# Kernel tuning notes

Measured on AMD Instinct MI355X. Metric: run time of the kernel, lower is better.

Reference implementation:

```python
import jax, jax.numpy as jnp
import numpy as np


def setup_inputs() -> dict:
    key = jax.random.key(0)
    k1, k2 = jax.random.split(key)
    B, N, T, D = 4, 5000, 96, 64
    spatial_nodes = jax.random.normal(k1, (B, N, D), dtype=jnp.float32)
    temporal_nodes = jax.random.normal(k2, (B, T, D), dtype=jnp.float32)
    return {"spatial_nodes": spatial_nodes, "temporal_nodes": temporal_nodes}


def reference(spatial_nodes, temporal_nodes):
    # node_embs: [B, N+T, D]
    node_embs = jnp.concatenate([spatial_nodes, temporal_nodes], axis=1)
    # Gram matrix per batch: [B, N+T, N+T]
    adj = jax.nn.relu(jnp.einsum('bnf,bmf->bnm', node_embs, node_embs))
    M = node_embs.shape[1]
    eye = jnp.eye(M, dtype=adj.dtype)  # broadcast over batch instead of repeat
    adj = jnp.tanh(adj + eye)
    # NOTE: the torch original additionally extracts per-batch edge lists via
    # adj[bi].nonzero() — a data-dependent-shape compaction that is not
    # jit-expressible; the dense adj carries identical information
    # (edge (i,j) exists iff adj[b,i,j] != 0, weight = adj[b,i,j]).
    return adj
```

## Files before the change

kernel.cpp:

```cpp
#include <hip/hip_runtime.h>


#define NSP 5000
#define NTM 96
#define MM  5096
#define DD  64
#define BT  128
#define NTILE 40

typedef __attribute__((ext_vector_type(8))) short short8;
typedef __attribute__((ext_vector_type(8))) unsigned short ushort8;
typedef __attribute__((ext_vector_type(4))) float f32x4;

#define OFF_RH 0u
#define OFF_RL 16384u
#define OFF_CH 32768u
#define OFF_CL 49152u

__device__ __forceinline__ unsigned short bf16_rn(float x) {
  unsigned u = __float_as_uint(x);
  u += 0x7FFFu + ((u >> 16) & 1u);
  return (unsigned short)(u >> 16);
}
__device__ __forceinline__ float bf16_f32(unsigned short s) {
  return __uint_as_float(((unsigned)s) << 16);
}

__global__ __launch_bounds__(256) void stg_adj_kernel(
    const float* __restrict__ sp, const float* __restrict__ tm,
    float* __restrict__ out) {
  __shared__ unsigned char lds[65536];
  const int bi = blockIdx.x;
  const int bj = blockIdx.y;
  const int b  = blockIdx.z;
  const int t  = threadIdx.x;

  {
    const int r = t >> 1;
    const int h = t & 1;
    #pragma unroll
    for (int side = 0; side < 2; ++side) {
      const int tbase = (side == 0 ? bi : bj) * BT;
      unsigned char* dh = lds + (side == 0 ? OFF_RH : OFF_CH);
      unsigned char* dl = lds + (side == 0 ? OFF_RL : OFF_CL);
      const int g = tbase + r;
      float f[32];
      if (g < MM) {
        const float* src = (g < NSP)
            ? sp + ((size_t)b * NSP + g) * DD + h * 32
            : tm + ((size_t)b * NTM + (g - NSP)) * DD + h * 32;
        const float4* s4 = reinterpret_cast<const float4*>(src);
        #pragma unroll
        for (int i = 0; i < 8; ++i) {
          float4 v = s4[i];
          f[4*i+0] = v.x; f[4*i+1] = v.y; f[4*i+2] = v.z; f[4*i+3] = v.w;
        }
      } else {
        #pragma unroll
        for (int i = 0; i < 32; ++i) f[i] = 0.f;
      }
      #pragma unroll
      for (int c = 0; c < 4; ++c) {
        ushort8 H, L;
        #pragma unroll
        for (int i = 0; i < 8; ++i) {
          const float x = f[8*c + i];
          const unsigned short hi = bf16_rn(x);
          H[i] = (unsigned short)hi;
          L[i] = bf16_rn(x - bf16_f32(hi));
        }
        const unsigned slot = (unsigned)(h * 4 + c);
        const unsigned byte = (unsigned)(r << 7) + ((slot << 4) ^ (((unsigned)(r & 7)) << 4));
        *reinterpret_cast<ushort8*>(dh + byte) = H;
        *reinterpret_cast<ushort8*>(dl + byte) = L;
      }
    }
  }
  __syncthreads();

  const int lane = t & 63;
  const int wave = t >> 6;
  const int wr = (wave >> 1) << 6;
  const int wc = (wave & 1) << 6;
  const int lr = lane & 15;
  const int lg = lane >> 4;

  f32x4 acc[4][4];
  #pragma unroll
  for (int m = 0; m < 4; ++m)
    #pragma unroll
    for (int n = 0; n < 4; ++n)
      acc[m][n] = (f32x4){0.f, 0.f, 0.f, 0.f};

  #pragma unroll
  for (int ks = 0; ks < 2; ++ks) {
    short8 ah[4], al[4], bh[4], bl[4];
    #pragma unroll
    for (int m = 0; m < 4; ++m) {
      const int rowa = wr + m * 16 + lr;
      const unsigned sa = ((unsigned)(lg + ks * 4)) << 4;
      const unsigned ba = (unsigned)(rowa << 7) + (sa ^ (((unsigned)(rowa & 7)) << 4));
      ah[m] = *reinterpret_cast<short8*>(lds + OFF_RH + ba);
      al[m] = *reinterpret_cast<short8*>(lds + OFF_RL + ba);
      const int rowb = wc + m * 16 + lr;
      const unsigned bb = (unsigned)(rowb << 7) + (sa ^ (((unsigned)(rowb & 7)) << 4));
      bh[m] = *reinterpret_cast<short8*>(lds + OFF_CH + bb);
      bl[m] = *reinterpret_cast<short8*>(lds + OFF_CL + bb);
    }
    #pragma unroll
    for (int m = 0; m < 4; ++m) {
      #pragma unroll
      for (int n = 0; n < 4; ++n) {
        acc[m][n] = __builtin_amdgcn_mfma_f32_16x16x32_bf16(ah[m], bh[n], acc[m][n], 0, 0, 0);
        acc[m][n] = __builtin_amdgcn_mfma_f32_16x16x32_bf16(ah[m], bl[n], acc[m][n], 0, 0, 0);
        acc[m][n] = __builtin_amdgcn_mfma_f32_16x16x32_bf16(al[m], bh[n], acc[m][n], 0, 0, 0);
      }
    }
  }

  const size_t cbase = (size_t)b * MM * MM;
  const int gr0 = bi * BT + wr;
  const int gc0 = bj * BT + wc;
  #pragma unroll
  for (int m = 0; m < 4; ++m) {
    #pragma unroll
    for (int n = 0; n < 4; ++n) {
      const int gc = gc0 + n * 16 + lr;
      #pragma unroll
      for (int q = 0; q < 4; ++q) {
        const int gr = gr0 + m * 16 + lg * 4 + q;
        if (gr < MM && gc < MM) {
          float x = acc[m][n][q];
          x = fmaxf(x, 0.f);
          if (gr == gc) x += 1.f;
          const float e = __builtin_amdgcn_exp2f(x * 2.8853900817779268f);
          out[cbase + (size_t)gr * MM + gc] = 1.f - 2.f * __builtin_amdgcn_rcpf(e + 1.f);
        }
      }
    }
  }
}

extern "C" void kernel_launch(void* const* d_in, const int* in_sizes, int n_in,
                              void* d_out, int out_size, void* d_ws, size_t ws_size,
                              hipStream_t stream) {
  const float* sp = (const float*)d_in[0];
  const float* tm = (const float*)d_in[1];
  float* out = (float*)d_out;
  const int B = in_sizes[0] / (NSP * DD);
  dim3 grid(NTILE, NTILE, B);
  stg_adj_kernel<<<grid, dim3(256), 0, stream>>>(sp, tm, out);
}
```

Before: 122.7 us.

## Precompute bf16 hi/lo split in prep kernel, load fragments directly, vectorize output stores

Adds a prep kernel that converts the concatenated inputs once into bf16 hi/lo arrays in workspace. The GEMM kernel then loads MFMA fragments straight from global memory instead of converting and staging through LDS, which removes the LDS traffic and the barrier. Swapping the MFMA operands transposes the accumulator layout, so each lane can write 4 contiguous floats as one nontemporal vector store instead of scattered scalar stores. The cost is an extra kernel launch, a workspace round trip, and redundant global fragment loads across tiles, which the cache is expected to absorb.

```diff
diff --git a/kernel.cpp b/kernel.cpp
--- a/kernel.cpp
+++ b/kernel.cpp
@@ -12,11 +12,6 @@
 typedef __attribute__((ext_vector_type(8))) unsigned short ushort8;
 typedef __attribute__((ext_vector_type(4))) float f32x4;
 
-#define OFF_RH 0u
-#define OFF_RL 16384u
-#define OFF_CH 32768u
-#define OFF_CL 49152u
-
 __device__ __forceinline__ unsigned short bf16_rn(float x) {
   unsigned u = __float_as_uint(x);
   u += 0x7FFFu + ((u >> 16) & 1u);
@@ -26,64 +21,65 @@
   return __uint_as_float(((unsigned)s) << 16);
 }
 
+__global__ __launch_bounds__(256) void stg_prep_kernel(
+    const float* __restrict__ sp, const float* __restrict__ tm,
+    unsigned short* __restrict__ wsh, unsigned short* __restrict__ wsl) {
+  const int tid = blockIdx.x * 256 + threadIdx.x;
+  const int flat = tid * 8;
+  const int b = flat / (MM * DD);
+  const int rem = flat - b * (MM * DD);
+  const int m = rem / DD;
+  const int d = rem - m * DD;
+  const float* src = (m < NSP)
+      ? sp + ((size_t)b * NSP + m) * DD + d
+      : tm + ((size_t)b * NTM + (m - NSP)) * DD + d;
+  const float4* s4 = reinterpret_cast<const float4*>(src);
+  float f[8];
+  {
+    float4 v0 = s4[0], v1 = s4[1];
+    f[0]=v0.x; f[1]=v0.y; f[2]=v0.z; f[3]=v0.w;
+    f[4]=v1.x; f[5]=v1.y; f[6]=v1.z; f[7]=v1.w;
+  }
+  ushort8 H, L;
+  #pragma unroll
+  for (int i = 0; i < 8; ++i) {
+    const unsigned short hi = bf16_rn(f[i]);
+    H[i] = hi;
+    L[i] = bf16_rn(f[i] - bf16_f32(hi));
+  }
+  *reinterpret_cast<ushort8*>(wsh + flat) = H;
+  *reinterpret_cast<ushort8*>(wsl + flat) = L;
+}
+
 __global__ __launch_bounds__(256) void stg_adj_kernel(
-    const float* __restrict__ sp, const float* __restrict__ tm,
+    const unsigned short* __restrict__ wsh,
+    const unsigned short* __restrict__ wsl,
     float* __restrict__ out) {
-  __shared__ unsigned char lds[65536];
   const int bi = blockIdx.x;
   const int bj = blockIdx.y;
   const int b  = blockIdx.z;
   const int t  = threadIdx.x;
-
-  {
-    const int r = t >> 1;
-    const int h = t & 1;
-    #pragma unroll
-    for (int side = 0; side < 2; ++side) {
-      const int tbase = (side == 0 ? bi : bj) * BT;
-      unsigned char* dh = lds + (side == 0 ? OFF_RH : OFF_CH);
-      unsigned char* dl = lds + (side == 0 ? OFF_RL : OFF_CL);
-      const int g = tbase + r;
-      float f[32];
-      if (g < MM) {
-        const float* src = (g < NSP)
-            ? sp + ((size_t)b * NSP + g) * DD + h * 32
-            : tm + ((size_t)b * NTM + (g - NSP)) * DD + h * 32;
-        const float4* s4 = reinterpret_cast<const float4*>(src);
-        #pragma unroll
-        for (int i = 0; i < 8; ++i) {
-          float4 v = s4[i];
-          f[4*i+0] = v.x; f[4*i+1] = v.y; f[4*i+2] = v.z; f[4*i+3] = v.w;
-        }
-      } else {
-        #pragma unroll
-        for (int i = 0; i < 32; ++i) f[i] = 0.f;
-      }
-      #pragma unroll
-      for (int c = 0; c < 4; ++c) {
-        ushort8 H, L;
-        #pragma unroll
-        for (int i = 0; i < 8; ++i) {
-          const float x = f[8*c + i];
-          const unsigned short hi = bf16_rn(x);
-          H[i] = (unsigned short)hi;
-          L[i] = bf16_rn(x - bf16_f32(hi));
-        }
-        const unsigned slot = (unsigned)(h * 4 + c);
-        const unsigned byte = (unsigned)(r << 7) + ((slot << 4) ^ (((unsigned)(r & 7)) << 4));
-        *reinterpret_cast<ushort8*>(dh + byte) = H;
-        *reinterpret_cast<ushort8*>(dl + byte) = L;
-      }
-    }
-  }
-  __syncthreads();
-
   const int lane = t & 63;
   const int wave = t >> 6;
   const int wr = (wave >> 1) << 6;
   const int wc = (wave & 1) << 6;
   const int lr = lane & 15;
   const int lg = lane >> 4;
+
+  const size_t pb = (size_t)b * MM * DD;
+  const char* Xh = reinterpret_cast<const char*>(wsh + pb);
+  const char* Xl = reinterpret_cast<const char*>(wsl + pb);
+  const int gr0 = bi * BT + wr;
+  const int gc0 = bj * BT + wc;
+
+  unsigned offr[4], offc[4];
+  #pragma unroll
+  for (int m = 0; m < 4; ++m) {
+    int rr = gr0 + m * 16 + lr; rr = rr < MM ? rr : MM - 1;
+    offr[m] = (unsigned)rr * 128u + (unsigned)lg * 16u;
+    int rc = gc0 + m * 16 + lr; rc = rc < MM ? rc : MM - 1;
+    offc[m] = (unsigned)rc * 128u + (unsigned)lg * 16u;
+  }
 
   f32x4 acc[4][4];
   #pragma unroll
@@ -94,48 +90,47 @@
 
   #pragma unroll
   for (int ks = 0; ks < 2; ++ks) {
-    short8 ah[4], al[4], bh[4], bl[4];
+    const unsigned ko = (unsigned)ks * 64u;
+    short8 rh[4], rl[4], ch[4], cl[4];
     #pragma unroll
     for (int m = 0; m < 4; ++m) {
-      const int rowa = wr + m * 16 + lr;
-      const unsigned sa = ((unsigned)(lg + ks * 4)) << 4;
-      const unsigned ba = (unsigned)(rowa << 7) + (sa ^ (((unsigned)(rowa & 7)) << 4));
-      ah[m] = *reinterpret_cast<short8*>(lds + OFF_RH + ba);
-      al[m] = *reinterpret_cast<short8*>(lds + OFF_RL + ba);
-      const int rowb = wc + m * 16 + lr;
-      const unsigned bb = (unsigned)(rowb << 7) + (sa ^ (((unsigned)(rowb & 7)) << 4));
-      bh[m] = *reinterpret_cast<short8*>(lds + OFF_CH + bb);
-      bl[m] = *reinterpret_cast<short8*>(lds + OFF_CL + bb);
+      rh[m] = *reinterpret_cast<const short8*>(Xh + offr[m] + ko);
+      rl[m] = *reinterpret_cast<const short8*>(Xl + offr[m] + ko);
+      ch[m] = *reinterpret_cast<const short8*>(Xh + offc[m] + ko);
+      cl[m] = *reinterpret_cast<const short8*>(Xl + offc[m] + ko);
     }
     #pragma unroll
     for (int m = 0; m < 4; ++m) {
       #pragma unroll
       for (int n = 0; n < 4; ++n) {
-        acc[m][n] = __builtin_amdgcn_mfma_f32_16x16x32_bf16(ah[m], bh[n], acc[m][n], 0, 0, 0);
-        acc[m][n] = __builtin_amdgcn_mfma_f32_16x16x32_bf16(ah[m], bl[n], acc[m][n], 0, 0, 0);
-        acc[m][n] = __builtin_amdgcn_mfma_f32_16x16x32_bf16(al[m], bh[n], acc[m][n], 0, 0, 0);
+        acc[m][n] = __builtin_amdgcn_mfma_f32_16x16x32_bf16(ch[n], rh[m], acc[m][n], 0, 0, 0);
+        acc[m][n] = __builtin_amdgcn_mfma_f32_16x16x32_bf16(ch[n], rl[m], acc[m][n], 0, 0, 0);
+        acc[m][n] = __builtin_amdgcn_mfma_f32_16x16x32_bf16(cl[n], rh[m], acc[m][n], 0, 0, 0);
       }
     }
   }
 
   const size_t cbase = (size_t)b * MM * MM;
-  const int gr0 = bi * BT + wr;
-  const int gc0 = bj * BT + wc;
+  int grs[4]; bool rv[4];
+  #pragma unroll
+  for (int m = 0; m < 4; ++m) { grs[m] = gr0 + m * 16 + lr; rv[m] = grs[m] < MM; }
+
   #pragma unroll
   for (int m = 0; m < 4; ++m) {
+    float* rowp = out + cbase + (size_t)grs[m] * MM;
     #pragma unroll
     for (int n = 0; n < 4; ++n) {
-      const int gc = gc0 + n * 16 + lr;
-      #pragma unroll
-      for (int q = 0; q < 4; ++q) {
-        const int gr = gr0 + m * 16 + lg * 4 + q;
-        if (gr < MM && gc < MM) {
-          float x = acc[m][n][q];
-          x = fmaxf(x, 0.f);
-          if (gr == gc) x += 1.f;
+      const int gc = gc0 + n * 16 + lg * 4;
+      if (rv[m] && gc < MM) {
+        f32x4 v;
+        #pragma unroll
+        for (int q = 0; q < 4; ++q) {
+          float x = fmaxf(acc[m][n][q], 0.f);
+          x += (grs[m] == gc + q) ? 1.f : 0.f;
           const float e = __builtin_amdgcn_exp2f(x * 2.8853900817779268f);
-          out[cbase + (size_t)gr * MM + gc] = 1.f - 2.f * __builtin_amdgcn_rcpf(e + 1.f);
+          v[q] = 1.f - 2.f * __builtin_amdgcn_rcpf(e + 1.f);
         }
+        __builtin_nontemporal_store(v, reinterpret_cast<f32x4*>(rowp + gc));
       }
     }
   }
@@ -148,6 +143,12 @@
   const float* tm = (const float*)d_in[1];
   float* out = (float*)d_out;
   const int B = in_sizes[0] / (NSP * DD);
+  unsigned short* wsh = (unsigned short*)d_ws;
+  unsigned short* wsl = wsh + (size_t)B * MM * DD;
+
+  const int prep_threads = B * MM * DD / 8;
+  stg_prep_kernel<<<dim3(prep_threads / 256), dim3(256), 0, stream>>>(sp, tm, wsh, wsl);
+
   dim3 grid(NTILE, NTILE, B);
-  stg_adj_kernel<<<grid, dim3(256), 0, stream>>>(sp, tm, out);
+  stg_adj_kernel<<<grid, dim3(256), 0, stream>>>(wsh, wsl, out);
 }
```

After: 286.0 us. 133% more time.
